# Kernel optimization log

Hardware: AMD Instinct MI355X
Metric: run time of the kernel (lower is better)

The kernel has to match this reference:

```python
import jax, jax.numpy as jnp
import numpy as np

N_NODES = 100000


def _gcn_layer(x, src, dst, deg_inv_sqrt, W, b):
    # GCNConv: out = D^{-1/2} (A + I) D^{-1/2} X W + b  (symmetric norm, self-loops)
    xw = x @ W  # [N, out]
    norm = deg_inv_sqrt[src] * deg_inv_sqrt[dst]  # [E]
    msg = xw[src] * norm[:, None]  # [E, out] gathered messages
    agg = jax.ops.segment_sum(msg, dst, num_segments=N_NODES)
    # self-loop contribution: norm_ii = deg_inv_sqrt[i]^2
    agg = agg + (deg_inv_sqrt * deg_inv_sqrt)[:, None] * xw
    return agg + b


def setup_inputs() -> dict:
    key = jax.random.key(0)
    k1, k2, k3, k4, k5, k6 = jax.random.split(key, 6)
    F_IN, HID, OUT, E = 128, 256, 40, 1600000
    x = jax.random.normal(k1, (N_NODES, F_IN), dtype=jnp.float32)
    edge_index = jax.random.randint(k2, (2, E), 0, N_NODES, dtype=jnp.int64)
    s1 = 1.0 / np.sqrt(F_IN)
    s2 = 1.0 / np.sqrt(HID)
    W1 = jax.random.uniform(k3, (F_IN, HID), jnp.float32, -s1, s1)
    b1 = jnp.zeros((HID,), jnp.float32)
    W2 = jax.random.uniform(k4, (HID, OUT), jnp.float32, -s2, s2)
    b2 = jnp.zeros((OUT,), jnp.float32)
    return {"x": x, "edge_index": edge_index, "W1": W1, "b1": b1, "W2": W2, "b2": b2}


def reference(x, edge_index, W1, b1, W2, b2):
    src, dst = edge_index[0], edge_index[1]
    # degree with self-loops (GCNConv default add_self_loops=True)
    deg = jax.ops.segment_sum(jnp.ones_like(dst, dtype=x.dtype), dst, num_segments=N_NODES) + 1.0
    deg_inv_sqrt = jax.lax.rsqrt(deg)
    h = _gcn_layer(x, src, dst, deg_inv_sqrt, W1, b1)
    h = jax.nn.relu(h)
    # dropout is identity in eval mode
    h = _gcn_layer(h, src, dst, deg_inv_sqrt, W2, b2)
    return jax.nn.log_softmax(h, axis=1)
```

## Files before the change

kernel.cpp:

```cpp
#include <hip/hip_runtime.h>
#include <math.h>

typedef long long ll;
typedef unsigned int uint;
typedef __attribute__((ext_vector_type(8))) short bf16x8;
typedef __attribute__((ext_vector_type(4))) float f32x4;

#define FIN 128
#define HID 256
#define FOUT 40
#define NG 8
#define NBIN 64

__device__ __forceinline__ float bflo(uint u) { return __uint_as_float(u << 16); }
__device__ __forceinline__ float bfhi(uint u) { return __uint_as_float(u & 0xFFFF0000u); }
__device__ __forceinline__ unsigned short f2bf(float f) {
  uint u = __float_as_uint(f);
  u += 0x7FFFu + ((u >> 16) & 1u);
  return (unsigned short)(u >> 16);
}

__device__ __forceinline__ int detect64(const uint* __restrict__ ei) {
  return (ei[1] == 0u && ei[3] == 0u && ei[5] == 0u && ei[7] == 0u) ? 1 : 0;
}

__global__ __launch_bounds__(256) void k_init(
    const void* __restrict__ ei, int* __restrict__ cnt,
    const float* __restrict__ W1, const float* __restrict__ W2,
    unsigned short* __restrict__ w1p, unsigned short* __restrict__ w2p,
    int2* __restrict__ pairs, int* __restrict__ hist, int n, ll E) {
  int i = blockIdx.x * 256 + threadIdx.x;
  int T = gridDim.x * 256;
  if (i < n) cnt[i] = 0;
  if (i < NBIN) hist[i] = 0;
  if (i < 32768) {
    int j = i & 7, g = (i >> 3) & 3, c = (i >> 5) & 255, s = i >> 13;
    int k = s * 32 + g * 8 + j;
    w1p[i] = f2bf(W1[(size_t)k * HID + c]);
  } else if (i < 32768 + 12288) {
    int i2 = i - 32768;
    int j = i2 & 7, g = (i2 >> 3) & 3, q = i2 >> 5;
    int c = q % 48, s = q / 48;
    int k = s * 32 + g * 8 + j;
    w2p[i2] = (c < FOUT) ? f2bf(W2[(size_t)k * FOUT + c]) : (unsigned short)0;
  }
  int is64 = detect64((const uint*)ei);
  for (ll base = (ll)i * 4; base < E; base += (ll)T * 4) {
    int m = (int)((E - base < 4) ? (E - base) : 4);
    int s[4], d[4];
    if (is64) {
      if (m == 4) {
        longlong2 a0 = *(const longlong2*)((const ll*)ei + base);
        longlong2 a1 = *(const longlong2*)((const ll*)ei + base + 2);
        longlong2 b0 = *(const longlong2*)((const ll*)ei + E + base);
        longlong2 b1 = *(const longlong2*)((const ll*)ei + E + base + 2);
        s[0]=(int)a0.x; s[1]=(int)a0.y; s[2]=(int)a1.x; s[3]=(int)a1.y;
        d[0]=(int)b0.x; d[1]=(int)b0.y; d[2]=(int)b1.x; d[3]=(int)b1.y;
      } else {
        for (int j = 0; j < m; ++j) { s[j]=(int)((const ll*)ei)[base+j]; d[j]=(int)((const ll*)ei)[E+base+j]; }
      }
    } else {
      if (m == 4) {
        int4 a = *(const int4*)((const int*)ei + base);
        int4 b = *(const int4*)((const int*)ei + E + base);
        s[0]=a.x; s[1]=a.y; s[2]=a.z; s[3]=a.w;
        d[0]=b.x; d[1]=b.y; d[2]=b.z; d[3]=b.w;
      } else {
        for (int j = 0; j < m; ++j) { s[j]=((const int*)ei)[base+j]; d[j]=((const int*)ei)[E+base+j]; }
      }
    }
    for (int j = 0; j < m; ++j) pairs[base + j] = make_int2(s[j], d[j]);
  }
}

__global__ __launch_bounds__(256) void k_count(
    const int2* __restrict__ pairs, int* __restrict__ cnt, ll E, int range, int n) {
  int g = blockIdx.x & (NG - 1);
  int lo = g * range;
  int hi = min(n, lo + range);
  ll tig = (ll)(blockIdx.x >> 3) * 256 + threadIdx.x;
  ll TIG = (ll)(gridDim.x >> 3) * 256;
  for (ll i = tig * 2; i < E; i += TIG * 2) {
    if (i + 1 < E) {
      int4 p = *(const int4*)(pairs + i);
      if (p.y >= lo && p.y < hi) atomicAdd(&cnt[p.y], 1);
      if (p.w >= lo && p.w < hi) atomicAdd(&cnt[p.w], 1);
    } else {
      int2 p = pairs[i];
      if (p.y >= lo && p.y < hi) atomicAdd(&cnt[p.y], 1);
    }
  }
}

__global__ __launch_bounds__(1024) void k_scan1(const int* __restrict__ cnt,
                                                int* __restrict__ row_off,
                                                int* __restrict__ blksums, int n) {
  __shared__ int sm[1024];
  int t = threadIdx.x;
  int base = blockIdx.x * 4096 + t * 4;
  int v0 = (base + 0 < n) ? cnt[base + 0] : 0;
  int v1 = (base + 1 < n) ? cnt[base + 1] : 0;
  int v2 = (base + 2 < n) ? cnt[base + 2] : 0;
  int v3 = (base + 3 < n) ? cnt[base + 3] : 0;
  int s = v0 + v1 + v2 + v3;
  sm[t] = s;
  __syncthreads();
  for (int off = 1; off < 1024; off <<= 1) {
    int u = (t >= off) ? sm[t - off] : 0;
    __syncthreads();
    sm[t] += u;
    __syncthreads();
  }
  int excl = sm[t] - s;
  if (base + 0 < n) row_off[base + 0] = excl;
  if (base + 1 < n) row_off[base + 1] = excl + v0;
  if (base + 2 < n) row_off[base + 2] = excl + v0 + v1;
  if (base + 3 < n) row_off[base + 3] = excl + v0 + v1 + v2;
  if (t == 1023) blksums[blockIdx.x] = sm[1023];
}

__global__ void k_scan2(int* __restrict__ blksums, int nb) {
  if (threadIdx.x == 0 && blockIdx.x == 0) {
    int acc = 0;
    for (int i = 0; i < nb; ++i) { int v = blksums[i]; blksums[i] = acc; acc += v; }
    blksums[nb] = acc;
  }
}

__global__ __launch_bounds__(1024) void k_scan3(
    int* __restrict__ row_off, int* __restrict__ cursor,
    const int* __restrict__ blksums, float* __restrict__ dis,
    int* __restrict__ hist, int n, int nb) {
  __shared__ int lh[NBIN];
  int t = threadIdx.x;
  if (t < NBIN) lh[t] = 0;
  __syncthreads();
  int i = blockIdx.x * 1024 + t;
  if (i < n) {
    int c = cursor[i];
    int v = row_off[i] + blksums[i >> 12];
    row_off[i] = v;
    cursor[i] = v;
    dis[i] = rsqrtf((float)c + 1.0f);
    atomicAdd(&lh[min(c, NBIN - 1)], 1);
  }
  if (i == 0) row_off[n] = blksums[nb];
  __syncthreads();
  if (t < NBIN && lh[t]) atomicAdd(&hist[t], lh[t]);
}

__global__ void k_binpfx(const int* __restrict__ hist, int* __restrict__ bincur) {
  if (threadIdx.x == 0 && blockIdx.x == 0) {
    int acc = 0;
    for (int b = 0; b < NBIN; ++b) { int v = hist[b]; bincur[b] = acc; acc += v; }
  }
}

__global__ __launch_bounds__(256) void k_perm(
    const int* __restrict__ row_off, int* __restrict__ bincur,
    int* __restrict__ perm, int n) {
  __shared__ int lh[NBIN], lbase[NBIN];
  int t = threadIdx.x;
  if (t < NBIN) lh[t] = 0;
  __syncthreads();
  int base = blockIdx.x * 4096 + t * 16;
  int deg[16];
  #pragma unroll
  for (int j = 0; j < 16; ++j) {
    int i = base + j;
    if (i < n) {
      deg[j] = min(row_off[i + 1] - row_off[i], NBIN - 1);
      atomicAdd(&lh[deg[j]], 1);
    } else deg[j] = -1;
  }
  __syncthreads();
  if (t < NBIN) {
    lbase[t] = lh[t] ? atomicAdd(&bincur[t], lh[t]) : 0;
    lh[t] = 0;
  }
  __syncthreads();
  #pragma unroll
  for (int j = 0; j < 16; ++j) {
    if (deg[j] >= 0) {
      int r = atomicAdd(&lh[deg[j]], 1);
      perm[lbase[deg[j]] + r] = base + j;
    }
  }
}

__global__ __launch_bounds__(256) void k_fill(
    const int2* __restrict__ pairs, int* __restrict__ cursor,
    int* __restrict__ csr, ll E, int range, int n) {
  int g = blockIdx.x & (NG - 1);
  int lo = g * range;
  int hi = min(n, lo + range);
  ll tig = (ll)(blockIdx.x >> 3) * 256 + threadIdx.x;
  ll TIG = (ll)(gridDim.x >> 3) * 256;
  for (ll i = tig * 2; i < E; i += TIG * 2) {
    if (i + 1 < E) {
      int4 p = *(const int4*)(pairs + i);
      if (p.y >= lo && p.y < hi) { int pos = atomicAdd(&cursor[p.y], 1); csr[pos] = p.x; }
      if (p.w >= lo && p.w < hi) { int pos = atomicAdd(&cursor[p.w], 1); csr[pos] = p.z; }
    } else {
      int2 p = pairs[i];
      if (p.y >= lo && p.y < hi) { int pos = atomicAdd(&cursor[p.y], 1); csr[pos] = p.x; }
    }
  }
}

__global__ __launch_bounds__(256) void k_xcast(
    const float* __restrict__ x, const float* __restrict__ dis,
    unsigned short* __restrict__ xb, int total8) {
  int i = blockIdx.x * 256 + threadIdx.x;
  if (i >= total8) return;
  float w = dis[i >> 4];
  const float4* p = (const float4*)x + (size_t)i * 2;
  float4 a = p[0], b = p[1];
  uint4 o;
  o.x = (uint)f2bf(w * a.x) | ((uint)f2bf(w * a.y) << 16);
  o.y = (uint)f2bf(w * a.z) | ((uint)f2bf(w * a.w) << 16);
  o.z = (uint)f2bf(w * b.x) | ((uint)f2bf(w * b.y) << 16);
  o.w = (uint)f2bf(w * b.z) | ((uint)f2bf(w * b.w) << 16);
  *(uint4*)(xb + (size_t)i * 8) = o;
}

__device__ __forceinline__ void add8(float* a, uint4 r) {
  a[0] += bflo(r.x); a[1] += bfhi(r.x);
  a[2] += bflo(r.y); a[3] += bfhi(r.y);
  a[4] += bflo(r.z); a[5] += bfhi(r.z);
  a[6] += bflo(r.w); a[7] += bfhi(r.w);
}

__global__ __launch_bounds__(256) void k_fused1(
    const unsigned short* __restrict__ xb, const int* __restrict__ csr,
    const int* __restrict__ row_off, const float* __restrict__ dis,
    const int* __restrict__ perm,
    const unsigned short* __restrict__ w1p, const float* __restrict__ b1,
    const unsigned short* __restrict__ w2p, unsigned short* __restrict__ xw2b,
    int n)
{
  __shared__ __align__(16) unsigned short xsb[16 * 136];
  __shared__ __align__(16) unsigned short hsb[16 * 264];
  __shared__ int   nid[16];
  __shared__ float dsh[16];

  int tid = threadIdx.x;
  int n0 = blockIdx.x * 16;
  int wv = tid >> 6, lane = tid & 63, qq = lane >> 4, l16 = lane & 15;
  int nl = wv * 4 + qq;
  int idx = n0 + nl;
  int node = (idx < n) ? perm[idx] : -1;

  float a[8] = {0, 0, 0, 0, 0, 0, 0, 0};
  float di = 0.f;
  if (node >= 0) {
    di = dis[node];
    uint4 v = *((const uint4*)(xb + (size_t)node * FIN) + l16);
    add8(a, v);
    int e0 = row_off[node], e1 = row_off[node + 1];
    int e = e0;
    for (; e + 8 <= e1; e += 8) {
      int s0 = csr[e],     s1 = csr[e + 1], s2 = csr[e + 2], s3 = csr[e + 3];
      int s4 = csr[e + 4], s5 = csr[e + 5], s6 = csr[e + 6], s7 = csr[e + 7];
      uint4 r0 = *((const uint4*)(xb + (size_t)s0 * FIN) + l16);
      uint4 r1 = *((const uint4*)(xb + (size_t)s1 * FIN) + l16);
      uint4 r2 = *((const uint4*)(xb + (size_t)s2 * FIN) + l16);
      uint4 r3 = *((const uint4*)(xb + (size_t)s3 * FIN) + l16);
      uint4 r4 = *((const uint4*)(xb + (size_t)s4 * FIN) + l16);
      uint4 r5 = *((const uint4*)(xb + (size_t)s5 * FIN) + l16);
      uint4 r6 = *((const uint4*)(xb + (size_t)s6 * FIN) + l16);
      uint4 r7 = *((const uint4*)(xb + (size_t)s7 * FIN) + l16);
      add8(a, r0); add8(a, r1); add8(a, r2); add8(a, r3);
      add8(a, r4); add8(a, r5); add8(a, r6); add8(a, r7);
    }
    for (; e < e1; ++e) {
      uint4 r0 = *((const uint4*)(xb + (size_t)csr[e] * FIN) + l16);
      add8(a, r0);
    }
  }
  if (l16 == 0) { nid[nl] = node; dsh[nl] = di; }
  {
    uint4 pk;
    pk.x = (uint)f2bf(di * a[0]) | ((uint)f2bf(di * a[1]) << 16);
    pk.y = (uint)f2bf(di * a[2]) | ((uint)f2bf(di * a[3]) << 16);
    pk.z = (uint)f2bf(di * a[4]) | ((uint)f2bf(di * a[5]) << 16);
    pk.w = (uint)f2bf(di * a[6]) | ((uint)f2bf(di * a[7]) << 16);
    *(uint4*)(xsb + nl * 136 + l16 * 8) = pk;
  }
  __syncthreads();

  int mrow = lane & 15, g = lane >> 4;
  f32x4 acc1[4] = {{0,0,0,0},{0,0,0,0},{0,0,0,0},{0,0,0,0}};
  #pragma unroll
  for (int s = 0; s < 4; ++s) {
    bf16x8 av = *(const bf16x8*)(xsb + mrow * 136 + s * 32 + g * 8);
    #pragma unroll
    for (int t = 0; t < 4; ++t) {
      int c = wv * 64 + t * 16 + mrow;
      bf16x8 bv = *(const bf16x8*)(w1p + (((size_t)(s * 256 + c) * 4 + g) << 3));
      acc1[t] = __builtin_amdgcn_mfma_f32_16x16x32_bf16(av, bv, acc1[t], 0, 0, 0);
    }
  }
  #pragma unroll
  for (int t = 0; t < 4; ++t) {
    int c = wv * 64 + t * 16 + mrow;
    float bb = b1[c];
    #pragma unroll
    for (int r = 0; r < 4; ++r) {
      float v = fmaxf(acc1[t][r] + bb, 0.f);
      hsb[(g * 4 + r) * 264 + c] = f2bf(v);
    }
  }
  __syncthreads();

  if (wv < 3) {
    f32x4 acc2 = {0, 0, 0, 0};
    int c2 = wv * 16 + mrow;
    #pragma unroll
    for (int s = 0; s < 8; ++s) {
      bf16x8 av = *(const bf16x8*)(hsb + mrow * 264 + s * 32 + g * 8);
      bf16x8 bv = *(const bf16x8*)(w2p + (((size_t)(s * 48 + c2) * 4 + g) << 3));
      acc2 = __builtin_amdgcn_mfma_f32_16x16x32_bf16(av, bv, acc2, 0, 0, 0);
    }
    if (c2 < FOUT) {
      #pragma unroll
      for (int r = 0; r < 4; ++r) {
        int nodeg = nid[g * 4 + r];
        if (nodeg >= 0)
          xw2b[((size_t)nodeg << 6) + c2] = f2bf(acc2[r] * dsh[g * 4 + r]);
      }
    }
  }
}

__global__ __launch_bounds__(256) void k_layer2(
    const unsigned short* __restrict__ xw2b, const int* __restrict__ csr,
    const int* __restrict__ row_off, const float* __restrict__ dis,
    const int* __restrict__ perm,
    const float* __restrict__ b2, float* __restrict__ out, int n)
{
  int tid = threadIdx.x;
  int idx = blockIdx.x * 16 + (tid >> 4);
  int l16 = tid & 15;
  if (idx >= n) return;
  int node = perm[idx];
  float di = dis[node];
  float a0, a1, a2, a3;
  {
    uint2 v = *((const uint2*)(xw2b + ((size_t)node << 6)) + l16);
    a0 = bflo(v.x); a1 = bfhi(v.x); a2 = bflo(v.y); a3 = bfhi(v.y);
  }
  int e0 = row_off[node], e1 = row_off[node + 1];
  int e = e0;
  for (; e + 8 <= e1; e += 8) {
    int s0 = csr[e],     s1 = csr[e + 1], s2 = csr[e + 2], s3 = csr[e + 3];
    int s4 = csr[e + 4], s5 = csr[e + 5], s6 = csr[e + 6], s7 = csr[e + 7];
    uint2 r0 = *((const uint2*)(xw2b + ((size_t)s0 << 6)) + l16);
    uint2 r1 = *((const uint2*)(xw2b + ((size_t)s1 << 6)) + l16);
    uint2 r2 = *((const uint2*)(xw2b + ((size_t)s2 << 6)) + l16);
    uint2 r3 = *((const uint2*)(xw2b + ((size_t)s3 << 6)) + l16);
    uint2 r4 = *((const uint2*)(xw2b + ((size_t)s4 << 6)) + l16);
    uint2 r5 = *((const uint2*)(xw2b + ((size_t)s5 << 6)) + l16);
    uint2 r6 = *((const uint2*)(xw2b + ((size_t)s6 << 6)) + l16);
    uint2 r7 = *((const uint2*)(xw2b + ((size_t)s7 << 6)) + l16);
    a0 += bflo(r0.x); a1 += bfhi(r0.x); a2 += bflo(r0.y); a3 += bfhi(r0.y);
    a0 += bflo(r1.x); a1 += bfhi(r1.x); a2 += bflo(r1.y); a3 += bfhi(r1.y);
    a0 += bflo(r2.x); a1 += bfhi(r2.x); a2 += bflo(r2.y); a3 += bfhi(r2.y);
    a0 += bflo(r3.x); a1 += bfhi(r3.x); a2 += bflo(r3.y); a3 += bfhi(r3.y);
    a0 += bflo(r4.x); a1 += bfhi(r4.x); a2 += bflo(r4.y); a3 += bfhi(r4.y);
    a0 += bflo(r5.x); a1 += bfhi(r5.x); a2 += bflo(r5.y); a3 += bfhi(r5.y);
    a0 += bflo(r6.x); a1 += bfhi(r6.x); a2 += bflo(r6.y); a3 += bfhi(r6.y);
    a0 += bflo(r7.x); a1 += bfhi(r7.x); a2 += bflo(r7.y); a3 += bfhi(r7.y);
  }
  for (; e < e1; ++e) {
    uint2 r0 = *((const uint2*)(xw2b + ((size_t)csr[e] << 6)) + l16);
    a0 += bflo(r0.x); a1 += bfhi(r0.x); a2 += bflo(r0.y); a3 += bfhi(r0.y);
  }
  bool act = (l16 < 10);
  float l0 = -INFINITY, l1 = -INFINITY, l2 = -INFINITY, l3 = -INFINITY;
  if (act) {
    float4 bv = *(const float4*)(b2 + l16 * 4);
    l0 = di * a0 + bv.x; l1 = di * a1 + bv.y;
    l2 = di * a2 + bv.z; l3 = di * a3 + bv.w;
  }
  float m = fmaxf(fmaxf(l0, l1), fmaxf(l2, l3));
  #pragma unroll
  for (int off = 8; off > 0; off >>= 1) m = fmaxf(m, __shfl_xor(m, off));
  float s = 0.f;
  if (act) s = expf(l0 - m) + expf(l1 - m) + expf(l2 - m) + expf(l3 - m);
  #pragma unroll
  for (int off = 8; off > 0; off >>= 1) s += __shfl_xor(s, off);
  if (act) {
    float ls = m + logf(s);
    float4 o = make_float4(l0 - ls, l1 - ls, l2 - ls, l3 - ls);
    *(float4*)(out + (size_t)node * FOUT + l16 * 4) = o;
  }
}

extern "C" void kernel_launch(void* const* d_in, const int* in_sizes, int n_in,
                              void* d_out, int out_size, void* d_ws, size_t ws_size,
                              hipStream_t stream) {
  const float* x  = (const float*)d_in[0];
  const void*  ei = d_in[1];
  const float* W1 = (const float*)d_in[2];
  const float* b1 = (const float*)d_in[3];
  const float* W2 = (const float*)d_in[4];
  const float* b2 = (const float*)d_in[5];
  float* out = (float*)d_out;

  int n = in_sizes[0] / FIN;
  ll  E = (ll)in_sizes[1] / 2;
  int nb = (n + 4095) / 4096;
  int range = (n + NG - 1) / NG;

  char* ws = (char*)d_ws;
  size_t off = 0;
  auto carve = [&](size_t bytes) -> char* {
    char* p = ws + off;
    off = (off + bytes + 255) & ~(size_t)255;
    return p;
  };
  int*   row_off = (int*)carve((size_t)(n + 1) * 4);
  int*   cursor  = (int*)carve((size_t)n * 4);
  int2*  pairs   = (int2*)carve((size_t)E * 8);
  int*   csr     = (int*)carve((size_t)E * 4);
  int*   blksums = (int*)carve(64 * 4);
  int*   hist    = (int*)carve(NBIN * 4);
  int*   bincur  = (int*)carve(NBIN * 4);
  int*   perm    = (int*)carve((size_t)n * 4);
  float* dis     = (float*)carve((size_t)n * 4);
  unsigned short* xb   = (unsigned short*)carve((size_t)n * FIN * 2);
  unsigned short* w1p  = (unsigned short*)carve(32768 * 2);
  unsigned short* w2p  = (unsigned short*)carve(12288 * 2);
  unsigned short* xw2b = (unsigned short*)carve((size_t)n * 64 * 2);
  (void)n_in; (void)out_size; (void)ws_size;

  int gn256 = (n + 255) / 256;
  int gx8   = (n * FIN / 8 + 255) / 256;
  int gt16  = (n + 15) / 16;
  int gperm = (n + 4095) / 4096;

  hipLaunchKernelGGL(k_init,  dim3(gn256), dim3(256), 0, stream,
                     ei, cursor, W1, W2, w1p, w2p, pairs, hist, n, E);
  hipLaunchKernelGGL(k_count, dim3(512), dim3(256), 0, stream, pairs, cursor, E, range, n);
  hipLaunchKernelGGL(k_scan1, dim3(nb), dim3(1024), 0, stream, cursor, row_off, blksums, n);
  hipLaunchKernelGGL(k_scan2, dim3(1), dim3(1), 0, stream, blksums, nb);
  hipLaunchKernelGGL(k_scan3, dim3((n + 1023) / 1024), dim3(1024), 0, stream,
                     row_off, cursor, blksums, dis, hist, n, nb);
  hipLaunchKernelGGL(k_binpfx, dim3(1), dim3(1), 0, stream, hist, bincur);
  hipLaunchKernelGGL(k_perm,  dim3(gperm), dim3(256), 0, stream, row_off, bincur, perm, n);
  hipLaunchKernelGGL(k_fill,  dim3(512), dim3(256), 0, stream, pairs, cursor, csr, E, range, n);
  hipLaunchKernelGGL(k_xcast, dim3(gx8), dim3(256), 0, stream, x, dis, xb, n * FIN / 8);
  hipLaunchKernelGGL(k_fused1, dim3(gt16), dim3(256), 0, stream,
                     xb, csr, row_off, dis, perm, w1p, b1, w2p, xw2b, n);
  hipLaunchKernelGGL(k_layer2, dim3(gt16), dim3(256), 0, stream,
                     xw2b, csr, row_off, dis, perm, b2, out, n);
}
```

Measured before the change: 302.3 us.

## Fuse degree counting into edge init and shrink layer-2 message stride

Degree counting now happens inside k_init with direct atomics while the edge pairs are written, so the separate k_count pass that re-read all pairs is gone. Counter zeroing moves to memset calls, pair stores are vectorised, and the k_init and k_fill grids are enlarged. The layer-2 bf16 message buffer drops from a 64-wide padded row to 40 columns, cutting gather bytes, with only the active lanes issuing loads. The trade is unpartitioned atomics, which lose the locality of the old destination-range grouping, and 80-byte rows that are no longer aligned to natural boundaries.

```diff
diff --git a/kernel.cpp b/kernel.cpp
--- a/kernel.cpp
+++ b/kernel.cpp
@@ -28,11 +28,9 @@
     const void* __restrict__ ei, int* __restrict__ cnt,
     const float* __restrict__ W1, const float* __restrict__ W2,
     unsigned short* __restrict__ w1p, unsigned short* __restrict__ w2p,
-    int2* __restrict__ pairs, int* __restrict__ hist, int n, ll E) {
+    int2* __restrict__ pairs, ll E) {
   int i = blockIdx.x * 256 + threadIdx.x;
   int T = gridDim.x * 256;
-  if (i < n) cnt[i] = 0;
-  if (i < NBIN) hist[i] = 0;
   if (i < 32768) {
     int j = i & 7, g = (i >> 3) & 3, c = (i >> 5) & 255, s = i >> 13;
     int k = s * 32 + g * 8 + j;
@@ -69,26 +67,13 @@
         for (int j = 0; j < m; ++j) { s[j]=((const int*)ei)[base+j]; d[j]=((const int*)ei)[E+base+j]; }
       }
     }
-    for (int j = 0; j < m; ++j) pairs[base + j] = make_int2(s[j], d[j]);
-  }
-}
-
-__global__ __launch_bounds__(256) void k_count(
-    const int2* __restrict__ pairs, int* __restrict__ cnt, ll E, int range, int n) {
-  int g = blockIdx.x & (NG - 1);
-  int lo = g * range;
-  int hi = min(n, lo + range);
-  ll tig = (ll)(blockIdx.x >> 3) * 256 + threadIdx.x;
-  ll TIG = (ll)(gridDim.x >> 3) * 256;
-  for (ll i = tig * 2; i < E; i += TIG * 2) {
-    if (i + 1 < E) {
-      int4 p = *(const int4*)(pairs + i);
-      if (p.y >= lo && p.y < hi) atomicAdd(&cnt[p.y], 1);
-      if (p.w >= lo && p.w < hi) atomicAdd(&cnt[p.w], 1);
+    if (m == 4) {
+      *(int4*)(pairs + base)     = make_int4(s[0], d[0], s[1], d[1]);
+      *(int4*)(pairs + base + 2) = make_int4(s[2], d[2], s[3], d[3]);
     } else {
-      int2 p = pairs[i];
-      if (p.y >= lo && p.y < hi) atomicAdd(&cnt[p.y], 1);
-    }
+      for (int j = 0; j < m; ++j) pairs[base + j] = make_int2(s[j], d[j]);
+    }
+    for (int j = 0; j < m; ++j) atomicAdd(&cnt[d[j]], 1);
   }
 }
 
@@ -327,7 +312,7 @@
       for (int r = 0; r < 4; ++r) {
         int nodeg = nid[g * 4 + r];
         if (nodeg >= 0)
-          xw2b[((size_t)nodeg << 6) + c2] = f2bf(acc2[r] * dsh[g * 4 + r]);
+          xw2b[(size_t)nodeg * FOUT + c2] = f2bf(acc2[r] * dsh[g * 4 + r]);
       }
     }
   }
@@ -345,9 +330,10 @@
   if (idx >= n) return;
   int node = perm[idx];
   float di = dis[node];
-  float a0, a1, a2, a3;
-  {
-    uint2 v = *((const uint2*)(xw2b + ((size_t)node << 6)) + l16);
+  bool act = (l16 < 10);
+  float a0 = 0.f, a1 = 0.f, a2 = 0.f, a3 = 0.f;
+  if (act) {
+    uint2 v = *((const uint2*)(xw2b + (size_t)node * FOUT) + l16);
     a0 = bflo(v.x); a1 = bfhi(v.x); a2 = bflo(v.y); a3 = bfhi(v.y);
   }
   int e0 = row_off[node], e1 = row_off[node + 1];
@@ -355,28 +341,32 @@
   for (; e + 8 <= e1; e += 8) {
     int s0 = csr[e],     s1 = csr[e + 1], s2 = csr[e + 2], s3 = csr[e + 3];
     int s4 = csr[e + 4], s5 = csr[e + 5], s6 = csr[e + 6], s7 = csr[e + 7];
-    uint2 r0 = *((const uint2*)(xw2b + ((size_t)s0 << 6)) + l16);
-    uint2 r1 = *((const uint2*)(xw2b + ((size_t)s1 << 6)) + l16);
-    uint2 r2 = *((const uint2*)(xw2b + ((size_t)s2 << 6)) + l16);
-    uint2 r3 = *((const uint2*)(xw2b + ((size_t)s3 << 6)) + l16);
-    uint2 r4 = *((const uint2*)(xw2b + ((size_t)s4 << 6)) + l16);
-    uint2 r5 = *((const uint2*)(xw2b + ((size_t)s5 << 6)) + l16);
-    uint2 r6 = *((const uint2*)(xw2b + ((size_t)s6 << 6)) + l16);
-    uint2 r7 = *((const uint2*)(xw2b + ((size_t)s7 << 6)) + l16);
-    a0 += bflo(r0.x); a1 += bfhi(r0.x); a2 += bflo(r0.y); a3 += bfhi(r0.y);
-    a0 += bflo(r1.x); a1 += bfhi(r1.x); a2 += bflo(r1.y); a3 += bfhi(r1.y);
-    a0 += bflo(r2.x); a1 += bfhi(r2.x); a2 += bflo(r2.y); a3 += bfhi(r2.y);
-    a0 += bflo(r3.x); a1 += bfhi(r3.x); a2 += bflo(r3.y); a3 += bfhi(r3.y);
-    a0 += bflo(r4.x); a1 += bfhi(r4.x); a2 += bflo(r4.y); a3 += bfhi(r4.y);
-    a0 += bflo(r5.x); a1 += bfhi(r5.x); a2 += bflo(r5.y); a3 += bfhi(r5.y);
-    a0 += bflo(r6.x); a1 += bfhi(r6.x); a2 += bflo(r6.y); a3 += bfhi(r6.y);
-    a0 += bflo(r7.x); a1 += bfhi(r7.x); a2 += bflo(r7.y); a3 += bfhi(r7.y);
+    if (act) {
+      uint2 r0 = *((const uint2*)(xw2b + (size_t)s0 * FOUT) + l16);
+      uint2 r1 = *((const uint2*)(xw2b + (size_t)s1 * FOUT) + l16);
+      uint2 r2 = *((const uint2*)(xw2b + (size_t)s2 * FOUT) + l16);
+      uint2 r3 = *((const uint2*)(xw2b + (size_t)s3 * FOUT) + l16);
+      uint2 r4 = *((const uint2*)(xw2b + (size_t)s4 * FOUT) + l16);
+      uint2 r5 = *((const uint2*)(xw2b + (size_t)s5 * FOUT) + l16);
+      uint2 r6 = *((const uint2*)(xw2b + (size_t)s6 * FOUT) + l16);
+      uint2 r7 = *((const uint2*)(xw2b + (size_t)s7 * FOUT) + l16);
+      a0 += bflo(r0.x); a1 += bfhi(r0.x); a2 += bflo(r0.y); a3 += bfhi(r0.y);
+      a0 += bflo(r1.x); a1 += bfhi(r1.x); a2 += bflo(r1.y); a3 += bfhi(r1.y);
+      a0 += bflo(r2.x); a1 += bfhi(r2.x); a2 += bflo(r2.y); a3 += bfhi(r2.y);
+      a0 += bflo(r3.x); a1 += bfhi(r3.x); a2 += bflo(r3.y); a3 += bfhi(r3.y);
+      a0 += bflo(r4.x); a1 += bfhi(r4.x); a2 += bflo(r4.y); a3 += bfhi(r4.y);
+      a0 += bflo(r5.x); a1 += bfhi(r5.x); a2 += bflo(r5.y); a3 += bfhi(r5.y);
+      a0 += bflo(r6.x); a1 += bfhi(r6.x); a2 += bflo(r6.y); a3 += bfhi(r6.y);
+      a0 += bflo(r7.x); a1 += bfhi(r7.x); a2 += bflo(r7.y); a3 += bfhi(r7.y);
+    }
   }
   for (; e < e1; ++e) {
-    uint2 r0 = *((const uint2*)(xw2b + ((size_t)csr[e] << 6)) + l16);
-    a0 += bflo(r0.x); a1 += bfhi(r0.x); a2 += bflo(r0.y); a3 += bfhi(r0.y);
-  }
-  bool act = (l16 < 10);
+    int s0 = csr[e];
+    if (act) {
+      uint2 r0 = *((const uint2*)(xw2b + (size_t)s0 * FOUT) + l16);
+      a0 += bflo(r0.x); a1 += bfhi(r0.x); a2 += bflo(r0.y); a3 += bfhi(r0.y);
+    }
+  }
   float l0 = -INFINITY, l1 = -INFINITY, l2 = -INFINITY, l3 = -INFINITY;
   if (act) {
     float4 bv = *(const float4*)(b2 + l16 * 4);
@@ -432,24 +422,25 @@
   unsigned short* xb   = (unsigned short*)carve((size_t)n * FIN * 2);
   unsigned short* w1p  = (unsigned short*)carve(32768 * 2);
   unsigned short* w2p  = (unsigned short*)carve(12288 * 2);
-  unsigned short* xw2b = (unsigned short*)carve((size_t)n * 64 * 2);
+  unsigned short* xw2b = (unsigned short*)carve((size_t)n * FOUT * 2);
   (void)n_in; (void)out_size; (void)ws_size;
 
-  int gn256 = (n + 255) / 256;
-  int gx8   = (n * FIN / 8 + 255) / 256;
-  int gt16  = (n + 15) / 16;
+  int gx8  = (n * FIN / 8 + 255) / 256;
+  int gt16 = (n + 15) / 16;
   int gperm = (n + 4095) / 4096;
 
-  hipLaunchKernelGGL(k_init,  dim3(gn256), dim3(256), 0, stream,
-                     ei, cursor, W1, W2, w1p, w2p, pairs, hist, n, E);
-  hipLaunchKernelGGL(k_count, dim3(512), dim3(256), 0, stream, pairs, cursor, E, range, n);
+  hipMemsetAsync(cursor, 0, (size_t)n * 4, stream);
+  hipMemsetAsync(hist, 0, NBIN * 4, stream);
+
+  hipLaunchKernelGGL(k_init,  dim3(2048), dim3(256), 0, stream,
+                     ei, cursor, W1, W2, w1p, w2p, pairs, E);
   hipLaunchKernelGGL(k_scan1, dim3(nb), dim3(1024), 0, stream, cursor, row_off, blksums, n);
   hipLaunchKernelGGL(k_scan2, dim3(1), dim3(1), 0, stream, blksums, nb);
   hipLaunchKernelGGL(k_scan3, dim3((n + 1023) / 1024), dim3(1024), 0, stream,
                      row_off, cursor, blksums, dis, hist, n, nb);
   hipLaunchKernelGGL(k_binpfx, dim3(1), dim3(1), 0, stream, hist, bincur);
   hipLaunchKernelGGL(k_perm,  dim3(gperm), dim3(256), 0, stream, row_off, bincur, perm, n);
-  hipLaunchKernelGGL(k_fill,  dim3(512), dim3(256), 0, stream, pairs, cursor, csr, E, range, n);
+  hipLaunchKernelGGL(k_fill,  dim3(2048), dim3(256), 0, stream, pairs, cursor, csr, E, range, n);
   hipLaunchKernelGGL(k_xcast, dim3(gx8), dim3(256), 0, stream, x, dis, xb, n * FIN / 8);
   hipLaunchKernelGGL(k_fused1, dim3(gt16), dim3(256), 0, stream,
                      xb, csr, row_off, dis, perm, w1p, b1, w2p, xw2b, n);
```

After: 300.9 us. About the same (-0.5%).
